# Kernel tuning notes

Measured on AMD Instinct MI355X. Metric: run time of the kernel, lower is better.

Reference implementation:

```python
import jax, jax.numpy as jnp
import jax.scipy.linalg as jsl
import numpy as np

EPS = 1e-7            # torchvision iou-loss eps
GIOU_THRESHOLD = 0.2
MIN_VARIANCE = 1e-6


def cxcywh_to_xyxy(b):
    cx, cy, w, h = b[..., 0], b[..., 1], b[..., 2], b[..., 3]
    return jnp.stack([cx - 0.5 * w, cy - 0.5 * h, cx + 0.5 * w, cy + 0.5 * h], axis=-1)


def kalman_filtered_boxes(prev_boxes, prev_logits, image_sizes, swp, sws, log_q_diag):
    # scale: [B,1,4] = [w,h,w,h] for denormalization
    scale = jnp.stack([image_sizes[:, 1], image_sizes[:, 0], image_sizes[:, 1], image_sizes[:, 0]], axis=-1)[:, None, :]
    box_abs = prev_boxes * scale                               # [B,Q,4] absolute cxcywh
    conf = jax.nn.softmax(prev_logits, axis=-1).max(axis=-1)   # [B,Q]
    # predict step: P_pred = F P0 F^T + Q  (track-independent 8x8)
    idx = jnp.arange(4)
    F = jnp.eye(8, dtype=box_abs.dtype).at[idx, idx + 4].set(1.0)
    P0 = jnp.diag(jnp.array([100.0] * 4 + [1000.0] * 4, dtype=box_abs.dtype))
    Qm = jnp.diag(jnp.exp(log_q_diag))
    P_pred = F @ P0 @ F.T + Qm                                 # [8,8]
    # detection covariance R per track (DetectionCovarianceGate)
    hc = jnp.maximum(box_abs[..., 3], 1.0)
    std = jnp.stack([swp * hc, swp * hc, sws * hc, sws * hc], axis=-1)
    std = std / jnp.maximum(conf, 1e-6)[..., None]
    std = jnp.maximum(std, 0.1)
    eye4 = jnp.eye(4, dtype=box_abs.dtype)
    R = eye4 * (std ** 2)[..., None, :] + MIN_VARIANCE * eye4  # [B,Q,4,4]
    # innovation covariance, gain via batched Cholesky + triangular solves
    S = P_pred[:4, :4] + R + MIN_VARIANCE * eye4               # [B,Q,4,4]
    L = jnp.linalg.cholesky(S)
    covHT_T = jnp.broadcast_to(P_pred[:, :4].T, S.shape[:-2] + (4, 8))
    y = jsl.solve_triangular(L, covHT_T, lower=True)
    Kt = jsl.solve_triangular(jnp.swapaxes(L, -1, -2), y, lower=False)
    K = jnp.swapaxes(Kt, -1, -2)                               # [B,Q,8,4]
    # state init from the same box + zero velocity -> F @ mean0 = [box; 0]
    mean_pred = jnp.concatenate([box_abs, jnp.zeros_like(box_abs)], axis=-1)  # [B,Q,8]
    innovation = box_abs - mean_pred[..., :4]  # identically zero; kept faithful to original
    mean_new = mean_pred + jnp.einsum('bqij,bqj->bqi', K, innovation)
    return mean_new[..., :4] / scale


def pairwise_giou_loss(p, t):
    # p: [B,Q,4], t: [B,T,4] in xyxy -> [B,Q,T] GIoU loss
    a = p[:, :, None, :]
    b = t[:, None, :, :]
    area_a = (a[..., 2] - a[..., 0]) * (a[..., 3] - a[..., 1])
    area_b = (b[..., 2] - b[..., 0]) * (b[..., 3] - b[..., 1])
    lt = jnp.maximum(a[..., :2], b[..., :2])
    rb = jnp.minimum(a[..., 2:], b[..., 2:])
    wh = jnp.maximum(rb - lt, 0.0)
    inter = wh[..., 0] * wh[..., 1]
    union = area_a + area_b - inter
    iou = inter / (union + EPS)
    ltc = jnp.minimum(a[..., :2], b[..., :2])
    rbc = jnp.maximum(a[..., 2:], b[..., 2:])
    whc = jnp.maximum(rbc - ltc, 0.0)
    area_c = whc[..., 0] * whc[..., 1]
    giou = iou - (area_c - union) / (area_c + EPS)
    return 1.0 - giou


def ciou_loss_mean(p, t):
    # elementwise complete-IoU loss (torchvision semantics), mean-reduced
    x1, y1, x2, y2 = p[..., 0], p[..., 1], p[..., 2], p[..., 3]
    xg1, yg1, xg2, yg2 = t[..., 0], t[..., 1], t[..., 2], t[..., 3]
    iw = jnp.maximum(jnp.minimum(x2, xg2) - jnp.maximum(x1, xg1), 0.0)
    ih = jnp.maximum(jnp.minimum(y2, yg2) - jnp.maximum(y1, yg1), 0.0)
    inter = iw * ih
    union = (x2 - x1) * (y2 - y1) + (xg2 - xg1) * (yg2 - yg1) - inter
    iou = inter / (union + EPS)
    cw = jnp.maximum(x2, xg2) - jnp.minimum(x1, xg1)
    ch = jnp.maximum(y2, yg2) - jnp.minimum(y1, yg1)
    c2 = cw ** 2 + ch ** 2 + EPS
    d2 = ((x1 + x2 - xg1 - xg2) ** 2 + (y1 + y2 - yg1 - yg2) ** 2) / 4.0
    v = (4.0 / (jnp.pi ** 2)) * (jnp.arctan((xg2 - xg1) / (yg2 - yg1)) - jnp.arctan((x2 - x1) / (y2 - y1))) ** 2
    alpha = jax.lax.stop_gradient(v / (1.0 - iou + v + EPS))
    return jnp.mean(1.0 - iou + d2 / c2 + alpha * v)


def _hungarian(cost):
    # O(n^3) shortest-augmenting-path Hungarian (min-cost square assignment).
    # Returns col assignment for rows 0..n-1 (rows are implicitly arange(n)).
    n = cost.shape[0]
    u = np.zeros(n + 1)
    v = np.zeros(n + 1)
    p = np.zeros(n + 1, dtype=np.int64)
    way = np.zeros(n + 1, dtype=np.int64)
    for i in range(1, n + 1):
        p[0] = i
        j0 = 0
        minv = np.full(n + 1, np.inf)
        used = np.zeros(n + 1, dtype=bool)
        while True:
            used[j0] = True
            i0 = p[j0]
            js = np.nonzero(~used)[0]
            js = js[js > 0]
            cur = cost[i0 - 1, js - 1] - u[i0] - v[js]
            upd = cur < minv[js]
            minv[js] = np.minimum(minv[js], cur)
            way[js[upd]] = j0
            j1 = js[int(np.argmin(minv[js]))]
            delta = minv[j1]
            uj = np.nonzero(used)[0]
            u[p[uj]] += delta
            v[uj] -= delta
            minv[js] -= delta
            j0 = j1
            if p[j0] == 0:
                break
        while j0 != 0:
            j1 = way[j0]
            p[j0] = p[j1]
            j0 = j1
    col_of_row = np.empty(n, dtype=np.int64)
    for j in range(1, n + 1):
        col_of_row[p[j] - 1] = j - 1
    return col_of_row


def setup_inputs() -> dict:
    key = jax.random.key(0)
    k = jax.random.split(key, 4)
    B, Q, C = 8, 512, 92
    prev_boxes = jax.random.uniform(k[0], (B, Q, 4), jnp.float32)
    prev_logits = jax.random.normal(k[1], (B, Q, C), jnp.float32)
    curr_boxes = jax.random.uniform(k[2], (B, Q, 4), jnp.float32)
    image_sizes = jax.random.uniform(k[3], (B, 2), jnp.float32) * 800.0 + 480.0
    return {
        'prev_boxes': prev_boxes,
        'prev_logits': prev_logits,
        'curr_boxes': curr_boxes,
        'image_sizes': image_sizes,
        'std_weight_position': jnp.asarray(0.05, jnp.float32),
        'std_weight_size': jnp.asarray(0.05, jnp.float32),
        'log_q_diag': jnp.log(jnp.array([0.01] * 4 + [1e-4] * 4, jnp.float32)),
    }


def reference(prev_boxes, prev_logits, curr_boxes, image_sizes, std_weight_position, std_weight_size, log_q_diag):
    filtered = kalman_filtered_boxes(prev_boxes, prev_logits, image_sizes,
                                     std_weight_position, std_weight_size, log_q_diag)
    # Hungarian matching on thresholded pairwise GIoU-loss cost (no-grad in original)
    gl = pairwise_giou_loss(cxcywh_to_xyxy(curr_boxes), cxcywh_to_xyxy(filtered))  # [B,Q,Q]
    cost = np.asarray(jax.lax.stop_gradient(gl) < GIOU_THRESHOLD, dtype=np.float64)
    cols = jnp.asarray(np.stack([_hungarian(cost[b]) for b in range(cost.shape[0])]))
    # original: matched_preds = pred[col_indices]; matched_targets = target[row_indices] (rows=arange)
    matched_preds = jnp.take_along_axis(curr_boxes, cols[..., None], axis=1)
    matched_targets = filtered
    return ciou_loss_mean(cxcywh_to_xyxy(matched_preds), cxcywh_to_xyxy(matched_targets))
```

## Files before the change

kernel.cpp:

```cpp
#include <hip/hip_runtime.h>
#include <stdint.h>
#include <math.h>

#define NB 8
#define NQ 512

typedef unsigned long long u64;

static __device__ __forceinline__ u64 getw8(const u64 (&a)[8], int w) {
    u64 r = 0ull;
#pragma unroll
    for (int k = 0; k < 8; k++) if (k == w) r = a[k];
    return r;
}
static __device__ __forceinline__ void setbit8(u64 (&a)[8], int c) {
    int w = c >> 6; u64 m = 1ull << (c & 63);
#pragma unroll
    for (int k = 0; k < 8; k++) if (k == w) a[k] |= m;
}
static __device__ __forceinline__ bool getbit8(const u64 (&a)[8], int c) {
    return (getw8(a, c >> 6) >> (c & 63)) & 1ull;
}

__global__ void cost_kernel(const float* __restrict__ prev_boxes,
                            const float* __restrict__ curr_boxes,
                            const float* __restrict__ image_sizes,
                            u64* __restrict__ cost,
                            float* __restrict__ out) {
#pragma clang fp contract(off)
    int t = blockIdx.x * blockDim.x + threadIdx.x;
    if (t == 0) out[0] = 0.f;
    int b = t >> 18;
    int rem = t & (NQ * NQ - 1);
    int i = rem >> 9;
    int j = rem & (NQ - 1);
    float4 cb = ((const float4*)curr_boxes)[(b << 9) + i];
    float ax = cb.x - 0.5f * cb.z, ay = cb.y - 0.5f * cb.w;
    float az = cb.x + 0.5f * cb.z, aw = cb.y + 0.5f * cb.w;
    float H = image_sizes[2 * b + 0];
    float W = image_sizes[2 * b + 1];
    float4 pb = ((const float4*)prev_boxes)[(b << 9) + j];
    float fcx = (pb.x * W) / W, fcy = (pb.y * H) / H;
    float fw  = (pb.z * W) / W, fh  = (pb.w * H) / H;
    float bx = fcx - 0.5f * fw, by = fcy - 0.5f * fh;
    float bz = fcx + 0.5f * fw, bw = fcy + 0.5f * fh;
    float area_a = (az - ax) * (aw - ay);
    float area_b = (bz - bx) * (bw - by);
    float ltx = fmaxf(ax, bx), lty = fmaxf(ay, by);
    float rbx = fminf(az, bz), rby = fminf(aw, bw);
    float w = fmaxf(rbx - ltx, 0.f), h = fmaxf(rby - lty, 0.f);
    float inter = w * h;
    float uni = area_a + area_b - inter;
    float iou = inter / (uni + 1e-7f);
    float lcx = fminf(ax, bx), lcy = fminf(ay, by);
    float rcx = fmaxf(az, bz), rcy = fmaxf(aw, bw);
    float wc = fmaxf(rcx - lcx, 0.f), hc = fmaxf(rcy - lcy, 0.f);
    float areac = wc * hc;
    float giou = iou - (areac - uni) / (areac + 1e-7f);
    float gl = 1.f - giou;
    u64 m = __ballot(gl < 0.2f);
    if ((threadIdx.x & 63) == 0)
        cost[((size_t)((b << 9) + i)) * 8 + (j >> 6)] = m;
}

__global__ __launch_bounds__(64, 1) void hungarian_kernel(
        const u64* __restrict__ cost,
        const float* __restrict__ prev_boxes,
        const float* __restrict__ curr_boxes,
        const float* __restrict__ image_sizes,
        float* __restrict__ out) {
    int b = blockIdx.x;
    int lane = threadIdx.x;
    __shared__ __align__(16) u64 costL[NQ * 8];
    __shared__ int p[NQ + 1];
    __shared__ int wayL[NQ + 1];
    __shared__ int u[NQ + 1];
    __shared__ int vv[NQ + 1];
    __shared__ int minvA[NQ + 1];
    __shared__ unsigned char used[NQ + 1];

    {
        const ulonglong2* src = (const ulonglong2*)(cost + (size_t)b * NQ * 8);
        ulonglong2* dst = (ulonglong2*)costL;
        for (int k = lane; k < NQ * 4; k += 64) dst[k] = src[k];
    }
    for (int k = lane; k <= NQ; k += 64) { p[k] = k; wayL[k] = 0; u[k] = 0; vv[k] = 0; }
    __syncthreads();

    u64 nzB[8], c0B[8], dgB[8], apB[8];
#pragma unroll
    for (int w = 0; w < 8; w++) {
        const u64* Zr = costL + (((w << 6) + lane) << 3);
        u64 o = 0ull;
#pragma unroll
        for (int k = 0; k < 8; k++) o |= Zr[k];
        nzB[w] = __ballot(o != 0ull);
        c0B[w] = __ballot((Zr[0] & 1ull) != 0ull);
        dgB[w] = __ballot(((Zr[w] >> lane) & 1ull) != 0ull);
        apB[w] = 0ull;
    }

    bool ownerNZ0 = false;
    int owner0 = 1;
    u64 Zc[8];
#pragma unroll
    for (int k = 0; k < 8; k++) Zc[k] = 0ull;
    int wIdx = 0;
    u64 bits = 0ull, pendMask = ~0ull;
    bool started = false;

    auto intW = [&](int w) -> u64 {
        u64 x = getw8(c0B, w) | getw8(dgB, w);
        if (ownerNZ0) x |= getw8(apB, w);
        return getw8(nzB, w) & x;
    };
    auto runGeneral = [&](int igen) {
        for (int j = igen; j <= NQ; j++) p[j] = 0;
        for (int i2 = igen; i2 <= NQ; i2++) {
            p[0] = i2;
            for (int j = 0; j <= NQ; j++) { minvA[j] = 0x7fffffff; used[j] = 0; }
            int j0 = 0;
            while (true) {
                used[j0] = 1;
                int i0 = p[j0];
                int ui0 = u[i0];
                const u64* rr = costL + ((size_t)(i0 - 1) << 3);
                int delta = 0x7fffffff, j1 = 0;
                for (int j = 1; j <= NQ; j++) {
                    if (!used[j]) {
                        int cbit = (int)((rr[(j - 1) >> 6] >> ((j - 1) & 63)) & 1ull);
                        int cur = cbit - ui0 - vv[j];
                        if (cur < minvA[j]) { minvA[j] = cur; wayL[j] = (i2 << 10) | j0; }
                        if (minvA[j] < delta) { delta = minvA[j]; j1 = j; }
                    }
                }
                for (int j = 0; j <= NQ; j++) {
                    if (used[j]) { u[p[j]] += delta; vv[j] -= delta; }
                    else minvA[j] -= delta;
                }
                j0 = j1;
                if (p[j0] == 0) break;
            }
            while (j0) {
                int wv = wayL[j0];
                int jn = ((wv >> 10) == i2) ? (wv & 1023) : 0;
                p[j0] = p[jn];
                j0 = jn;
            }
        }
    };

    for (;;) {
        int action = 0;
        if (lane == 0) {
            if (!started) {
                started = true;
                if (nzB[0] & 1ull) {
                    u64 Z1[8];
#pragma unroll
                    for (int k = 0; k < 8; k++) Z1[k] = costL[k];
                    if (!(Z1[0] & 1ull)) {
                        owner0 = 1; ownerNZ0 = true;
#pragma unroll
                        for (int k = 0; k < 8; k++) Zc[k] = Z1[k];
                        action = 1; pendMask = ~1ull; wIdx = 0;
                    } else {
                        runGeneral(1); action = 3;
                    }
                } else {
                    bits = intW(0) & ~1ull;
                }
            }
            while (action == 0) {
                if (bits == 0ull) {
                    wIdx++;
                    if (wIdx >= 8) { action = 3; break; }
                    bits = intW(wIdx);
                    continue;
                }
                int l = __builtin_ctzll(bits);
                bits &= bits - 1;
                u64 rem = (l == 63) ? 0ull : (~0ull << (l + 1));
                int i = (wIdx << 6) + l + 1;
                bool c0 = (getw8(c0B, wIdx) >> l) & 1ull;
                bool apb = ownerNZ0 && ((getw8(apB, wIdx) >> l) & 1ull);
                if (!c0 && !apb) {
                    p[i] = owner0;
                    p[1] = i;
                    owner0 = i; ownerNZ0 = true;
#pragma unroll
                    for (int k = 0; k < 8; k++) Zc[k] = costL[((i - 1) << 3) + k];
                    action = 1; pendMask = rem;
                } else {
                    int prevO = owner0; bool prevF = ownerNZ0;
                    bool bail = false, hole = false;
                    u64 Z[8];
#pragma unroll
                    for (int k = 0; k < 8; k++) Z[k] = costL[((i - 1) << 3) + k];
                    u64 ones[8], vis[8], nzA[8], nzBf[8];
#pragma unroll
                    for (int k = 0; k < 8; k++) { ones[k] = Z[k]; vis[k] = 0ull; nzA[k] = 0ull; nzBf[k] = 0ull; }
                    int fA_c = 0, fA_p = 0, fB_c = 0, fB_p = 0;
                    int foldn = 0, assignTo = -1;
                    while (true) {
                        int c2 = -1;
#pragma unroll
                        for (int k = 7; k >= 0; k--) {
                            u64 s = ~ones[k] & ~vis[k];
                            if (s != 0ull) c2 = (k << 6) + __builtin_ctzll(s);
                        }
                        if (c2 < 0) { bail = true; break; }
                        if (c2 >= i - 1) {
                            if (c2 == i - 1) assignTo = c2;
                            else hole = true;
                            break;
                        }
                        int pc = p[c2 + 1];
                        u64 Zo[8];
#pragma unroll
                        for (int k = 0; k < 8; k++) Zo[k] = costL[((pc - 1) << 3) + k];
                        setbit8(vis, c2);
                        u64 nzv[8], ap2 = 0ull;
#pragma unroll
                        for (int k = 0; k < 8; k++) { nzv[k] = ones[k] & ~Zo[k]; ones[k] &= Zo[k]; ap2 |= ones[k]; }
                        if (foldn == 0) {
                            fA_c = c2; fA_p = pc;
#pragma unroll
                            for (int k = 0; k < 8; k++) nzA[k] = nzv[k];
                        } else if (foldn == 1) {
                            fB_c = c2; fB_p = pc;
#pragma unroll
                            for (int k = 0; k < 8; k++) nzBf[k] = nzv[k];
                        } else {
#pragma unroll
                            for (int k = 0; k < 8; k++) {
                                u64 tt = nzv[k];
                                while (tt) { int b2 = __builtin_ctzll(tt); tt &= tt - 1; wayL[(k << 6) + b2 + 1] = (i << 10) | (c2 + 1); }
                            }
                        }
                        foldn++;
                        if (ap2 == 0ull) { assignTo = i - 1; break; }
                    }
                    if (bail || hole) {
                        runGeneral(i);
                        action = 3;
                    } else {
                        int cc = assignTo;
                        while (true) {
                            bool inA = getbit8(nzA, cc), inB = getbit8(nzBf, cc);
                            if (inB)      { p[cc + 1] = fB_p; cc = fB_c; }
                            else if (inA) { p[cc + 1] = fA_p; cc = fA_c; }
                            else if (foldn > 2) {
                                int wv = wayL[cc + 1];
                                if ((wv >> 10) == i) { int jn = wv & 1023; p[cc + 1] = p[jn]; cc = jn - 1; }
                                else                 { p[cc + 1] = i; break; }
                            } else { p[cc + 1] = i; break; }
                        }
                        owner0 = p[1];
                        ownerNZ0 = (getw8(nzB, (owner0 - 1) >> 6) >> ((owner0 - 1) & 63)) & 1ull;
                        if (ownerNZ0 && !(prevF && prevO == owner0)) {
#pragma unroll
                            for (int k = 0; k < 8; k++) Zc[k] = costL[((owner0 - 1) << 3) + k];
                            action = 1; pendMask = rem;
                        } else {
                            bits = intW(wIdx) & rem;
                        }
                    }
                }
            }
        }
        action = __shfl(action, 0, 64);
        if (action == 1) {
            u64 zc[8];
#pragma unroll
            for (int k = 0; k < 8; k++) {
                int lo = __shfl((int)(Zc[k] & 0xffffffffull), 0, 64);
                int hi = __shfl((int)(Zc[k] >> 32), 0, 64);
                zc[k] = (((u64)(unsigned)hi) << 32) | (u64)(unsigned)lo;
            }
#pragma unroll
            for (int w = 0; w < 8; w++) {
                const u64* Zr = costL + (((w << 6) + lane) << 3);
                u64 a = 0ull;
#pragma unroll
                for (int k = 0; k < 8; k++) a |= Zr[k] & zc[k];
                apB[w] = __ballot(a != 0ull);
            }
            if (lane == 0) {
                ownerNZ0 = true;
                bits = intW(wIdx) & pendMask;
            }
            continue;
        }
        break;
    }
    __syncthreads();

    {
#pragma clang fp contract(off)
        float H = image_sizes[2 * b + 0];
        float W = image_sizes[2 * b + 1];
        float sum = 0.f;
#pragma unroll
        for (int k = 0; k < 8; k++) {
            int j = 1 + lane + (k << 6);
            int r = p[j] - 1;
            int c = j - 1;
            float4 cb = ((const float4*)curr_boxes)[(b << 9) + c];
            float x1 = cb.x - 0.5f * cb.z, y1 = cb.y - 0.5f * cb.w;
            float x2 = cb.x + 0.5f * cb.z, y2 = cb.y + 0.5f * cb.w;
            float4 pb = ((const float4*)prev_boxes)[(b << 9) + r];
            float fcx = (pb.x * W) / W, fcy = (pb.y * H) / H;
            float fw2 = (pb.z * W) / W, fh2 = (pb.w * H) / H;
            float xg1 = fcx - 0.5f * fw2, yg1 = fcy - 0.5f * fh2;
            float xg2 = fcx + 0.5f * fw2, yg2 = fcy + 0.5f * fh2;
            float iw = fmaxf(fminf(x2, xg2) - fmaxf(x1, xg1), 0.f);
            float ih = fmaxf(fminf(y2, yg2) - fmaxf(y1, yg1), 0.f);
            float inter = iw * ih;
            float uni = (x2 - x1) * (y2 - y1) + (xg2 - xg1) * (yg2 - yg1) - inter;
            float iou = inter / (uni + 1e-7f);
            float cw2 = fmaxf(x2, xg2) - fminf(x1, xg1);
            float ch2 = fmaxf(y2, yg2) - fminf(y1, yg1);
            float c2 = cw2 * cw2 + ch2 * ch2 + 1e-7f;
            float dx = ((x1 + x2) - xg1) - xg2;
            float dy = ((y1 + y2) - yg1) - yg2;
            float d2 = (dx * dx + dy * dy) / 4.f;
            const float CC = (float)(4.0 / (M_PI * M_PI));
            float at = atanf((xg2 - xg1) / (yg2 - yg1)) - atanf((x2 - x1) / (y2 - y1));
            float v = CC * (at * at);
            float alpha = v / (((1.f - iou) + v) + 1e-7f);
            sum += ((1.f - iou) + d2 / c2) + alpha * v;
        }
#pragma unroll
        for (int off = 32; off >= 1; off >>= 1) sum += __shfl_xor(sum, off, 64);
        if (lane == 0) atomicAdd(out, sum * (1.f / 4096.f));
    }
}

extern "C" void kernel_launch(void* const* d_in, const int* in_sizes, int n_in,
                              void* d_out, int out_size, void* d_ws, size_t ws_size,
                              hipStream_t stream) {
    const float* prev_boxes  = (const float*)d_in[0];
    const float* curr_boxes  = (const float*)d_in[2];
    const float* image_sizes = (const float*)d_in[3];

    u64* cost = (u64*)d_ws;
    float* out = (float*)d_out;

    cost_kernel<<<(NB * NQ * NQ) / 256, 256, 0, stream>>>(
        prev_boxes, curr_boxes, image_sizes, cost, out);
    hungarian_kernel<<<NB, 64, 0, stream>>>(
        cost, prev_boxes, curr_boxes, image_sizes, out);
}
```

Baseline: 91.51 us.

## Spread Hungarian bitmask scans across four wavefronts per batch block

The Hungarian kernel now runs with 256 threads (four wavefronts) per batch instead of one. Each wavefront computes two of the eight column-group ballots, both for the initial nonzero/diagonal masks and for the per-augment adjacency masks. Results are exchanged through shared memory, and thread 0 keeps the serial control logic. This shortens the parallel scan phases but replaces wavefront shuffles with block-wide __syncthreads barriers on every loop iteration, which may cost more than it saves when the serial part dominates.

```diff
diff --git a/kernel.cpp b/kernel.cpp
--- a/kernel.cpp
+++ b/kernel.cpp
@@ -63,14 +63,16 @@
         cost[((size_t)((b << 9) + i)) * 8 + (j >> 6)] = m;
 }
 
-__global__ __launch_bounds__(64, 1) void hungarian_kernel(
+__global__ __launch_bounds__(256, 1) void hungarian_kernel(
         const u64* __restrict__ cost,
         const float* __restrict__ prev_boxes,
         const float* __restrict__ curr_boxes,
         const float* __restrict__ image_sizes,
         float* __restrict__ out) {
     int b = blockIdx.x;
-    int lane = threadIdx.x;
+    int tid = threadIdx.x;
+    int lane = tid & 63;
+    int wv = tid >> 6;
     __shared__ __align__(16) u64 costL[NQ * 8];
     __shared__ int p[NQ + 1];
     __shared__ int wayL[NQ + 1];
@@ -78,36 +80,42 @@
     __shared__ int vv[NQ + 1];
     __shared__ int minvA[NQ + 1];
     __shared__ unsigned char used[NQ + 1];
+    __shared__ u64 nzS[8], c0S[8], dgS[8], apS[8], zcS[8];
+    __shared__ int actionS;
 
     {
         const ulonglong2* src = (const ulonglong2*)(cost + (size_t)b * NQ * 8);
         ulonglong2* dst = (ulonglong2*)costL;
-        for (int k = lane; k < NQ * 4; k += 64) dst[k] = src[k];
-    }
-    for (int k = lane; k <= NQ; k += 64) { p[k] = k; wayL[k] = 0; u[k] = 0; vv[k] = 0; }
+        for (int k = tid; k < NQ * 4; k += 256) dst[k] = src[k];
+    }
+    for (int k = tid; k <= NQ; k += 256) { p[k] = k; wayL[k] = 0; u[k] = 0; vv[k] = 0; }
     __syncthreads();
 
+#pragma unroll
+    for (int gi = 0; gi < 2; gi++) {
+        int g = 2 * wv + gi;
+        const u64* Zr = costL + (((g << 6) + lane) << 3);
+        u64 o = 0ull;
+#pragma unroll
+        for (int k = 0; k < 8; k++) o |= Zr[k];
+        u64 nzb = __ballot(o != 0ull);
+        u64 c0b = __ballot((Zr[0] & 1ull) != 0ull);
+        u64 dgb = __ballot(((Zr[g] >> lane) & 1ull) != 0ull);
+        if (lane == 0) { nzS[g] = nzb; c0S[g] = c0b; dgS[g] = dgb; apS[g] = 0ull; }
+    }
+    __syncthreads();
+
     u64 nzB[8], c0B[8], dgB[8], apB[8];
-#pragma unroll
-    for (int w = 0; w < 8; w++) {
-        const u64* Zr = costL + (((w << 6) + lane) << 3);
-        u64 o = 0ull;
-#pragma unroll
-        for (int k = 0; k < 8; k++) o |= Zr[k];
-        nzB[w] = __ballot(o != 0ull);
-        c0B[w] = __ballot((Zr[0] & 1ull) != 0ull);
-        dgB[w] = __ballot(((Zr[w] >> lane) & 1ull) != 0ull);
-        apB[w] = 0ull;
-    }
-
     bool ownerNZ0 = false;
     int owner0 = 1;
     u64 Zc[8];
-#pragma unroll
-    for (int k = 0; k < 8; k++) Zc[k] = 0ull;
     int wIdx = 0;
     u64 bits = 0ull, pendMask = ~0ull;
     bool started = false;
+    if (tid == 0) {
+#pragma unroll
+        for (int k = 0; k < 8; k++) { nzB[k] = nzS[k]; c0B[k] = c0S[k]; dgB[k] = dgS[k]; apB[k] = 0ull; Zc[k] = 0ull; }
+    }
 
     auto intW = [&](int w) -> u64 {
         u64 x = getw8(c0B, w) | getw8(dgB, w);
@@ -142,8 +150,8 @@
                 if (p[j0] == 0) break;
             }
             while (j0) {
-                int wv = wayL[j0];
-                int jn = ((wv >> 10) == i2) ? (wv & 1023) : 0;
+                int wv2 = wayL[j0];
+                int jn = ((wv2 >> 10) == i2) ? (wv2 & 1023) : 0;
                 p[j0] = p[jn];
                 j0 = jn;
             }
@@ -151,8 +159,8 @@
     };
 
     for (;;) {
-        int action = 0;
-        if (lane == 0) {
+        if (tid == 0) {
+            int action = 0;
             if (!started) {
                 started = true;
                 if (nzB[0] & 1ull) {
@@ -251,9 +259,9 @@
                             if (inB)      { p[cc + 1] = fB_p; cc = fB_c; }
                             else if (inA) { p[cc + 1] = fA_p; cc = fA_c; }
                             else if (foldn > 2) {
-                                int wv = wayL[cc + 1];
-                                if ((wv >> 10) == i) { int jn = wv & 1023; p[cc + 1] = p[jn]; cc = jn - 1; }
-                                else                 { p[cc + 1] = i; break; }
+                                int wv2 = wayL[cc + 1];
+                                if ((wv2 >> 10) == i) { int jn = wv2 & 1023; p[cc + 1] = p[jn]; cc = jn - 1; }
+                                else                  { p[cc + 1] = i; break; }
                             } else { p[cc + 1] = i; break; }
                         }
                         owner0 = p[1];
@@ -268,25 +276,32 @@
                     }
                 }
             }
+            if (action == 1) {
+#pragma unroll
+                for (int k = 0; k < 8; k++) zcS[k] = Zc[k];
+            }
+            actionS = action;
         }
-        action = __shfl(action, 0, 64);
+        __syncthreads();
+        int action = actionS;
         if (action == 1) {
             u64 zc[8];
 #pragma unroll
-            for (int k = 0; k < 8; k++) {
-                int lo = __shfl((int)(Zc[k] & 0xffffffffull), 0, 64);
-                int hi = __shfl((int)(Zc[k] >> 32), 0, 64);
-                zc[k] = (((u64)(unsigned)hi) << 32) | (u64)(unsigned)lo;
-            }
-#pragma unroll
-            for (int w = 0; w < 8; w++) {
-                const u64* Zr = costL + (((w << 6) + lane) << 3);
+            for (int k = 0; k < 8; k++) zc[k] = zcS[k];
+#pragma unroll
+            for (int gi = 0; gi < 2; gi++) {
+                int g = 2 * wv + gi;
+                const u64* Zr = costL + (((g << 6) + lane) << 3);
                 u64 a = 0ull;
 #pragma unroll
                 for (int k = 0; k < 8; k++) a |= Zr[k] & zc[k];
-                apB[w] = __ballot(a != 0ull);
-            }
-            if (lane == 0) {
+                u64 bal = __ballot(a != 0ull);
+                if (lane == 0) apS[g] = bal;
+            }
+            __syncthreads();
+            if (tid == 0) {
+#pragma unroll
+                for (int k = 0; k < 8; k++) apB[k] = apS[k];
                 ownerNZ0 = true;
                 bits = intW(wIdx) & pendMask;
             }
@@ -302,8 +317,8 @@
         float W = image_sizes[2 * b + 1];
         float sum = 0.f;
 #pragma unroll
-        for (int k = 0; k < 8; k++) {
-            int j = 1 + lane + (k << 6);
+        for (int k = 0; k < 2; k++) {
+            int j = 1 + tid + (k << 8);
             int r = p[j] - 1;
             int c = j - 1;
             float4 cb = ((const float4*)curr_boxes)[(b << 9) + c];
@@ -349,6 +364,6 @@
 
     cost_kernel<<<(NB * NQ * NQ) / 256, 256, 0, stream>>>(
         prev_boxes, curr_boxes, image_sizes, cost, out);
-    hungarian_kernel<<<NB, 64, 0, stream>>>(
+    hungarian_kernel<<<NB, 256, 0, stream>>>(
         cost, prev_boxes, curr_boxes, image_sizes, out);
 }
```

Result: faster. 79.49 us (-13.1%).
